# Optimization experiments

Hardware: AMD Instinct MI355X
Metric: run time of the kernel (lower is better)

The kernel has to match this reference:

```python
import jax, jax.numpy as jnp
import numpy as np

B, S, H = 4, 1024, 1024
NH, HD = 16, 64
SCALE = 1.0 / np.sqrt(HD)
VERB_BIAS, ROOT_BIAS, SUFFIX_BIAS = 2.0, 1.5, 1.2
BIG = np.float32(1e9)


def setup_inputs() -> dict:
    key = jax.random.key(0)
    ks = jax.random.split(key, 10)
    inp = {
        "hidden_states": jax.random.normal(ks[0], (B, S, H), dtype=jnp.float32),
        "morpho_types": jax.random.randint(ks[1], (B, S), 0, 5, dtype=jnp.int32),
        # torch Linear: y = x @ W.T + b; store W already transposed as [in, out]
        "Wq": jax.random.normal(ks[2], (H, H), dtype=jnp.float32) * 0.02,
        "bq": jnp.zeros((H,), dtype=jnp.float32),
        "Wk": jax.random.normal(ks[3], (H, H), dtype=jnp.float32) * 0.02,
        "bk": jnp.zeros((H,), dtype=jnp.float32),
        "Wv": jax.random.normal(ks[4], (H, H), dtype=jnp.float32) * 0.02,
        "bv": jnp.zeros((H,), dtype=jnp.float32),
        "Wo": jax.random.normal(ks[5], (H, H), dtype=jnp.float32) * 0.02,
        "bo": jnp.zeros((H,), dtype=jnp.float32),
    }
    return inp


def _morpho_bias(morpho_types):
    """Vectorized equivalent of _create_morpho_bias_mask. Returns [B, S, S]
    (the torch version broadcasts the same bias over all heads)."""
    is_verb = morpho_types == 2                      # [B, S]
    pos = jnp.arange(S)
    dist = jnp.abs(pos[:, None] - pos[None, :])      # [S, S]
    # mask non-verb columns with a huge distance; argmin ties -> smallest j,
    # matching torch's argmin over ascending verb_positions
    dist_m = jnp.where(is_verb[:, None, :], dist[None], BIG)  # [B, S, S]
    nearest = jnp.argmin(dist_m, axis=-1)            # [B, S]
    has_verb = jnp.any(is_verb, axis=-1)             # [B]
    verb_term = VERB_BIAS * jax.nn.one_hot(nearest, S, dtype=jnp.float32)
    verb_term = verb_term * has_verb[:, None, None].astype(jnp.float32)
    col_bias = (ROOT_BIAS * 0.5) * (morpho_types == 0).astype(jnp.float32) \
             + (SUFFIX_BIAS * 0.3) * (morpho_types == 1).astype(jnp.float32)  # [B, S]
    return verb_term + col_bias[:, None, :]          # [B, S, S]


def reference(hidden_states, morpho_types, Wq, bq, Wk, bk, Wv, bv, Wo, bo):
    def proj(W, b):
        y = hidden_states @ W + b                    # [B, S, H]
        return y.reshape(B, S, NH, HD).transpose(0, 2, 1, 3)  # [B, NH, S, HD]

    q = proj(Wq, bq)
    k = proj(Wk, bk)
    v = proj(Wv, bv)

    scores = jnp.einsum('bhqd,bhkd->bhqk', q, k) * SCALE   # [B, NH, S, S]
    scores = scores + _morpho_bias(morpho_types)[:, None]  # broadcast heads

    attn = jax.nn.softmax(scores, axis=-1)
    out = jnp.einsum('bhqk,bhkd->bhqd', attn, v)           # [B, NH, S, HD]
    out = out.transpose(0, 2, 1, 3).reshape(B, S, H)
    return out @ Wo + bo
```

## Files before the change

### kernel.cpp

```cpp
#include <hip/hip_runtime.h>


#define QSCALE 0.18033688011112042f
#define CB0    1.0820212806667225f
#define CB1    0.5193702147200268f
#define VERB2  2.8853900817779268f

typedef float  f32x4   __attribute__((ext_vector_type(4)));
typedef short  s16x8   __attribute__((ext_vector_type(8)));
typedef unsigned short u16x4 __attribute__((ext_vector_type(4)));
typedef unsigned short u16x8 __attribute__((ext_vector_type(8)));

#if __has_builtin(__builtin_amdgcn_exp2f)
#define EXP2F(x) __builtin_amdgcn_exp2f(x)
#else
#define EXP2F(x) exp2f(x)
#endif

__device__ __forceinline__ unsigned short f2bf(float f) {
  union { float f; unsigned u; } a; a.f = f;
  unsigned r = a.u + 0x7fffu + ((a.u >> 16) & 1u);
  return (unsigned short)(r >> 16);
}

__device__ __forceinline__ void async16(const void* g, void* l) {
  __builtin_amdgcn_global_load_lds(
      (const __attribute__((address_space(1))) unsigned int*)g,
      (__attribute__((address_space(3))) unsigned int*)l, 16, 0, 0);
}

__global__ __launch_bounds__(256) void k_prep(
    const float* __restrict__ hs, unsigned short* __restrict__ hsb,
    const float* __restrict__ Wq, const float* __restrict__ Wk,
    const float* __restrict__ Wv, const float* __restrict__ Wo,
    unsigned short* __restrict__ Wt, const int* __restrict__ mt,
    float* __restrict__ colbias, int* __restrict__ nearest) {
  __shared__ float t[64 * 68];
  int bx = blockIdx.x, tid = threadIdx.x;
  if (bx < 2048) {
    int i = (bx * 256 + tid) * 8;
    float4 v0 = *(const float4*)(hs + i);
    float4 v1 = *(const float4*)(hs + i + 4);
    u16x8 o;
    o[0] = f2bf(v0.x); o[1] = f2bf(v0.y); o[2] = f2bf(v0.z); o[3] = f2bf(v0.w);
    o[4] = f2bf(v1.x); o[5] = f2bf(v1.y); o[6] = f2bf(v1.z); o[7] = f2bf(v1.w);
    *(u16x8*)(hsb + i) = o;
  } else if (bx < 3072) {
    int w = (bx - 2048) >> 8, tt = (bx - 2048) & 255;
    const float* W = (w == 0) ? Wq : (w == 1) ? Wk : (w == 2) ? Wv : Wo;
    unsigned short* Wd = Wt + (size_t)w * 1048576;
    int n0 = (tt & 15) * 64, k0 = (tt >> 4) * 64;
    int r = tid >> 2, c0 = (tid & 3) * 16;
    const float* src = &W[(k0 + r) * 1024 + n0 + c0];
    float4 a0 = *(const float4*)(src + 0);
    float4 a1 = *(const float4*)(src + 4);
    float4 a2 = *(const float4*)(src + 8);
    float4 a3 = *(const float4*)(src + 12);
    *(float4*)&t[r * 68 + c0 + 0]  = a0;
    *(float4*)&t[r * 68 + c0 + 4]  = a1;
    *(float4*)&t[r * 68 + c0 + 8]  = a2;
    *(float4*)&t[r * 68 + c0 + 12] = a3;
    __syncthreads();
    u16x8 o0, o1;
#pragma unroll
    for (int j = 0; j < 8; j++) {
      o0[j] = f2bf(t[(c0 + j) * 68 + r]);
      o1[j] = f2bf(t[(c0 + 8 + j) * 68 + r]);
    }
    *(u16x8*)&Wd[(n0 + r) * 1024 + k0 + c0]     = o0;
    *(u16x8*)&Wd[(n0 + r) * 1024 + k0 + c0 + 8] = o1;
  } else {
    int i = bx - 3072;
    int b = i >> 2;
    int* sm = (int*)t;
    for (int j = tid; j < 1024; j += 256) sm[j] = mt[b * 1024 + j];
    __syncthreads();
    int q = (i & 3) * 256 + tid;
    int best = 1 << 30, bj = -1;
    for (int j = 0; j < 1024; ++j) {
      int d = (q > j) ? (q - j) : (j - q);
      int dd = (sm[j] == 2) ? d : (1 << 30);
      if (dd < best) { best = dd; bj = j; }
    }
    nearest[b * 1024 + q] = bj;
    int m = sm[q];
    colbias[b * 1024 + q] = CB0 * (m == 0) + CB1 * (m == 1);
  }
}

template <int MODE>
__global__ __launch_bounds__(256) void k_gemm(
    const unsigned short* __restrict__ A,
    const unsigned short* __restrict__ WtBase,
    const float* __restrict__ bias0, const float* __restrict__ bias1,
    const float* __restrict__ bias2,
    unsigned short* __restrict__ outB, unsigned short* __restrict__ outV,
    float* __restrict__ outF) {
  constexpr int TM = (MODE == 0) ? 128 : 64;
  constexpr int NI = (MODE == 0) ? 4 : 2;
  constexpr int RA = TM / 4;
  __shared__ unsigned short As[TM * 64];
  __shared__ unsigned short Bs[128 * 64];
  int tid = threadIdx.x, wid = tid >> 6, lane = tid & 63;
  int c = lane & 15, quad = lane >> 4;
  int m0, wsel, n0;
  const unsigned short* Bt;
  const float* bias;
  if (MODE == 0) {
    wsel = blockIdx.x >> 3;
    n0 = (blockIdx.x & 7) * 128;
    m0 = blockIdx.y * 128;
    Bt = WtBase + wsel * 1048576;
    bias = (wsel == 0) ? bias0 : ((wsel == 1) ? bias1 : bias2);
  } else {
    wsel = 0;
    n0 = blockIdx.x * 128;
    m0 = blockIdx.y * 64;
    Bt = WtBase; bias = bias0;
  }
  int wm = (wid >> 1) * (16 * NI), wn = (wid & 1) * 64;
  int lr = lane >> 3, lc = lane & 7;
  int gcol = ((lc ^ lr) << 3);
  const unsigned short* ga = A  + (size_t)(m0 + wid * RA + lr) * 1024 + gcol;
  const unsigned short* gb = Bt + (size_t)(n0 + wid * 32 + lr) * 1024 + gcol;
  unsigned short* lA = &As[(wid * RA) * 64];
  unsigned short* lB = &Bs[(wid * 32) * 64];

  f32x4 acc[NI][4];
#pragma unroll
  for (int i = 0; i < NI; i++)
#pragma unroll
    for (int j = 0; j < 4; j++) acc[i][j] = (f32x4){0.f, 0.f, 0.f, 0.f};

  bool sw = (MODE == 1) || (wsel != 2);

  for (int k0 = 0; k0 < 1024; k0 += 64) {
#pragma unroll
    for (int i = 0; i < RA / 8; i++) async16(ga + i * 8 * 1024 + k0, lA + i * 8 * 64);
#pragma unroll
    for (int j = 0; j < 4; j++)      async16(gb + j * 8 * 1024 + k0, lB + j * 8 * 64);
    __syncthreads();
#pragma unroll
    for (int ks = 0; ks < 2; ks++) {
      s16x8 af[NI], bf[4];
#pragma unroll
      for (int i = 0; i < NI; i++)
        af[i] = *(const s16x8*)&As[(wm + i * 16 + c) * 64 + (((ks * 4 + quad) ^ (c & 7)) << 3)];
#pragma unroll
      for (int j = 0; j < 4; j++)
        bf[j] = *(const s16x8*)&Bs[(wn + j * 16 + c) * 64 + (((ks * 4 + quad) ^ (c & 7)) << 3)];
      if (sw) {
#pragma unroll
        for (int i = 0; i < NI; i++)
#pragma unroll
          for (int j = 0; j < 4; j++)
            acc[i][j] = __builtin_amdgcn_mfma_f32_16x16x32_bf16(bf[j], af[i], acc[i][j], 0, 0, 0);
      } else {
#pragma unroll
        for (int i = 0; i < NI; i++)
#pragma unroll
          for (int j = 0; j < 4; j++)
            acc[i][j] = __builtin_amdgcn_mfma_f32_16x16x32_bf16(af[i], bf[j], acc[i][j], 0, 0, 0);
      }
    }
    __syncthreads();
  }

  if (MODE == 1) {
#pragma unroll
    for (int j = 0; j < 4; j++) {
      int colb = n0 + wn + j * 16 + quad * 4;
      f32x4 bvv = *(const f32x4*)&bias[colb];
#pragma unroll
      for (int i = 0; i < NI; i++) {
        int s_tok = m0 + wm + i * 16 + c;
        f32x4 v = acc[i][j] + bvv;
        *(f32x4*)&outF[(size_t)s_tok * 1024 + colb] = v;
      }
    }
  } else if (wsel == 2) {
#pragma unroll
    for (int j = 0; j < 4; j++) {
      int col = n0 + wn + j * 16 + c;
      float bv = bias[col];
      int h = col >> 6, d = col & 63;
#pragma unroll
      for (int i = 0; i < NI; i++) {
        int row = m0 + wm + i * 16 + quad * 4;
        int bb = row >> 10, s = row & 1023;
        u16x4 pk;
#pragma unroll
        for (int r = 0; r < 4; r++) pk[r] = f2bf(acc[i][j][r] + bv);
        *(u16x4*)&outV[(size_t)(((bb * 16 + h) * 64 + d)) * 1024 + s] = pk;
      }
    }
  } else {
    float sc = (wsel == 0) ? QSCALE : 1.0f;
#pragma unroll
    for (int j = 0; j < 4; j++) {
      int colb = n0 + wn + j * 16 + quad * 4;
      f32x4 bvv = *(const f32x4*)&bias[colb];
      int h = colb >> 6, d0 = colb & 63;
#pragma unroll
      for (int i = 0; i < NI; i++) {
        int s_tok = m0 + wm + i * 16 + c;
        int bb = s_tok >> 10, s = s_tok & 1023;
        u16x4 pk;
#pragma unroll
        for (int r = 0; r < 4; r++) pk[r] = f2bf((acc[i][j][r] + bvv[r]) * sc);
        *(u16x4*)&outB[(size_t)wsel * 4194304 + (((bb * 16 + h) * 1024 + s) * 64) + d0] = pk;
      }
    }
  }
}

__global__ __launch_bounds__(256) void k_attn(
    const unsigned short* __restrict__ Q, const unsigned short* __restrict__ K,
    const unsigned short* __restrict__ Vt, const float* __restrict__ colbias,
    const int* __restrict__ nearest, unsigned short* __restrict__ AO) {
  __shared__ unsigned short Ks[64 * 72];
  __shared__ unsigned short Vs[64 * 72];
  __shared__ unsigned short Ps[4][16 * 72];
  __shared__ float Cb[1024];
  int tid = threadIdx.x, wid = tid >> 6, lane = tid & 63;
  int c = lane & 15, quad = lane >> 4;
  int bh = blockIdx.x, qt = blockIdx.y;
  int b = bh >> 4, head = bh & 15;
  int q0 = qt * 64, wq = wid * 16;
  const unsigned short* Qg = Q  + (size_t)(bh * 1024 + q0 + wq) * 64;
  const unsigned short* Kg = K  + (size_t)bh * 1024 * 64;
  const unsigned short* Vg = Vt + (size_t)bh * 64 * 1024;

  *(float4*)&Cb[tid * 4] = *(const float4*)&colbias[b * 1024 + tid * 4];

  s16x8 qf[2];
#pragma unroll
  for (int ks = 0; ks < 2; ks++)
    qf[ks] = *(const s16x8*)&Qg[c * 64 + ks * 32 + quad * 8];

  int nq = nearest[b * 1024 + q0 + wq + c];

  f32x4 o[4];
#pragma unroll
  for (int j = 0; j < 4; j++) o[j] = (f32x4){0.f, 0.f, 0.f, 0.f};
  float lrun = 0.f;

  int srow = tid >> 3, scol8 = (tid & 7) * 8;

  u16x8 kr[2], vr[2];
#pragma unroll
  for (int it = 0; it < 2; ++it) {
    int r2 = it * 32 + srow;
    kr[it] = *(const u16x8*)&Kg[r2 * 64 + scol8];
    vr[it] = *(const u16x8*)&Vg[r2 * 1024 + scol8];
  }
  __syncthreads();

  for (int kc = 0; kc < 16; ++kc) {
#pragma unroll
    for (int it = 0; it < 2; ++it) {
      int r2 = it * 32 + srow;
      *(u16x8*)&Ks[r2 * 72 + scol8] = kr[it];
      *(u16x8*)&Vs[r2 * 72 + scol8] = vr[it];
    }
    __syncthreads();
    if (kc < 15) {
#pragma unroll
      for (int it = 0; it < 2; ++it) {
        int r2 = it * 32 + srow;
        kr[it] = *(const u16x8*)&Kg[((kc + 1) * 64 + r2) * 64 + scol8];
        vr[it] = *(const u16x8*)&Vg[r2 * 1024 + (kc + 1) * 64 + scol8];
      }
    }

    f32x4 st[4];
#pragma unroll
    for (int mt = 0; mt < 4; mt++) st[mt] = (f32x4){0.f, 0.f, 0.f, 0.f};
#pragma unroll
    for (int mt = 0; mt < 4; mt++)
#pragma unroll
      for (int ks = 0; ks < 2; ks++) {
        s16x8 a = *(const s16x8*)&Ks[(mt * 16 + c) * 72 + ks * 32 + quad * 8];
        st[mt] = __builtin_amdgcn_mfma_f32_16x16x32_bf16(a, qf[ks], st[mt], 0, 0, 0);
      }

    if (__any((nq >> 6) == kc)) {
#pragma unroll
      for (int mt = 0; mt < 4; mt++)
#pragma unroll
        for (int r = 0; r < 4; r++)
          if (kc * 64 + mt * 16 + quad * 4 + r == nq) st[mt][r] += VERB2;
    }

#pragma unroll
    for (int mt = 0; mt < 4; mt++) {
      f32x4 cb = *(const f32x4*)&Cb[kc * 64 + mt * 16 + quad * 4];
      float e0 = EXP2F(st[mt][0] + cb[0]);
      float e1 = EXP2F(st[mt][1] + cb[1]);
      float e2 = EXP2F(st[mt][2] + cb[2]);
      float e3 = EXP2F(st[mt][3] + cb[3]);
      unsigned p01 = __builtin_amdgcn_perm(__float_as_uint(e1), __float_as_uint(e0), 0x07060302u);
      unsigned p23 = __builtin_amdgcn_perm(__float_as_uint(e3), __float_as_uint(e2), 0x07060302u);
      lrun += __uint_as_float(p01 << 16) + __uint_as_float(p01 & 0xffff0000u)
            + __uint_as_float(p23 << 16) + __uint_as_float(p23 & 0xffff0000u);
      uint2 pk; pk.x = p01; pk.y = p23;
      *(uint2*)&Ps[wid][c * 72 + mt * 16 + quad * 4] = pk;
    }
    __asm__ volatile("s_waitcnt lgkmcnt(0)" ::: "memory");

#pragma unroll
    for (int ks = 0; ks < 2; ks++) {
      s16x8 pa = *(const s16x8*)&Ps[wid][c * 72 + ks * 32 + quad * 8];
#pragma unroll
      for (int ntd = 0; ntd < 4; ntd++) {
        s16x8 vb = *(const s16x8*)&Vs[(ntd * 16 + c) * 72 + ks * 32 + quad * 8];
        o[ntd] = __builtin_amdgcn_mfma_f32_16x16x32_bf16(vb, pa, o[ntd], 0, 0, 0);
      }
    }
    __syncthreads();
  }

  lrun += __shfl_xor(lrun, 16, 64);
  lrun += __shfl_xor(lrun, 32, 64);
  float linv = 1.0f / lrun;
  size_t row = (size_t)(b * 1024 + q0 + wq + c);
#pragma unroll
  for (int ntd = 0; ntd < 4; ntd++) {
    int d0 = ntd * 16 + quad * 4;
    u16x4 pk;
#pragma unroll
    for (int r = 0; r < 4; r++) pk[r] = f2bf(o[ntd][r] * linv);
    *(u16x4*)&AO[row * 1024 + head * 64 + d0] = pk;
  }
}

extern "C" void kernel_launch(void* const* d_in, const int* in_sizes, int n_in,
                              void* d_out, int out_size, void* d_ws, size_t ws_size,
                              hipStream_t stream) {
  const float* hs     = (const float*)d_in[0];
  const int*   morpho = (const int*)d_in[1];
  const float* Wq = (const float*)d_in[2];
  const float* bq = (const float*)d_in[3];
  const float* Wk = (const float*)d_in[4];
  const float* bk = (const float*)d_in[5];
  const float* Wv = (const float*)d_in[6];
  const float* bv = (const float*)d_in[7];
  const float* Wo = (const float*)d_in[8];
  const float* bo = (const float*)d_in[9];
  float* out = (float*)d_out;

  char* ws = (char*)d_ws;
  unsigned short* hsb = (unsigned short*)(ws);
  unsigned short* Wt  = (unsigned short*)(ws + (8u << 20));
  unsigned short* Qb  = (unsigned short*)(ws + (16u << 20));
  unsigned short* Kb  = (unsigned short*)(ws + (24u << 20));
  unsigned short* Vtb = (unsigned short*)(ws + (40u << 20));
  float* colbias      = (float*)(ws + (48u << 20));
  int*   nearestp     = (int*)(ws + (48u << 20) + (16u << 10));
  unsigned short* AO  = hsb;

  k_prep<<<3088, 256, 0, stream>>>(hs, hsb, Wq, Wk, Wv, Wo, Wt, morpho,
                                   colbias, nearestp);
  k_gemm<0><<<dim3(24, 32), 256, 0, stream>>>(hsb, Wt, bq, bk, bv, Qb, Vtb, nullptr);
  k_attn<<<dim3(64, 16), 256, 0, stream>>>(Qb, Kb, Vtb, colbias, nearestp, AO);
  k_gemm<1><<<dim3(8, 64), 256, 0, stream>>>(AO, Wt + 3 * 1048576, bo, nullptr, nullptr,
                                             nullptr, nullptr, out);
  (void)in_sizes; (void)n_in; (void)out_size; (void)ws_size; (void)Kb;
}
```

Baseline: 211.5 us.

## Double-buffer K/V LDS tiles in attention and stage output GEMM stores through LDS

The attention kernel now keeps two LDS buffers for K and V. Each iteration writes the next chunk into the alternate buffer and prefetches the chunk after that into registers, which drops the barrier that used to sit between the LDS store and the compute. The output-projection GEMM epilogue now transposes its accumulator tile through XOR-swizzled shared memory, so each wave writes full contiguous 256-byte rows to global memory instead of scattered 16-byte pieces. This costs more LDS for attention, which may lower occupancy. The single end-of-loop barrier must still protect the buffer being overwritten, and the rotation is subtle.

```diff
diff --git a/kernel.cpp b/kernel.cpp
--- a/kernel.cpp
+++ b/kernel.cpp
@@ -99,8 +99,9 @@
   constexpr int TM = (MODE == 0) ? 128 : 64;
   constexpr int NI = (MODE == 0) ? 4 : 2;
   constexpr int RA = TM / 4;
-  __shared__ unsigned short As[TM * 64];
-  __shared__ unsigned short Bs[128 * 64];
+  __shared__ unsigned short SMEM[16384];
+  unsigned short* As = SMEM;
+  unsigned short* Bs = SMEM + TM * 64;
   int tid = threadIdx.x, wid = tid >> 6, lane = tid & 63;
   int c = lane & 15, quad = lane >> 4;
   int m0, wsel, n0;
@@ -167,16 +168,27 @@
   }
 
   if (MODE == 1) {
+    float* Wf = (float*)SMEM + wid * 2048;
 #pragma unroll
     for (int j = 0; j < 4; j++) {
       int colb = n0 + wn + j * 16 + quad * 4;
       f32x4 bvv = *(const f32x4*)&bias[colb];
 #pragma unroll
       for (int i = 0; i < NI; i++) {
-        int s_tok = m0 + wm + i * 16 + c;
         f32x4 v = acc[i][j] + bvv;
-        *(f32x4*)&outF[(size_t)s_tok * 1024 + colb] = v;
-      }
+        int tokl = i * 16 + c;
+        int chs = (j * 4 + quad) ^ c;
+        *(f32x4*)&Wf[tokl * 64 + chs * 4] = v;
+      }
+    }
+    __asm__ volatile("s_waitcnt lgkmcnt(0)" ::: "memory");
+    int t4 = lane >> 4, chl = lane & 15;
+#pragma unroll
+    for (int t = 0; t < 8; t++) {
+      int tokl = t * 4 + t4;
+      int chs = chl ^ (tokl & 15);
+      f32x4 v = *(const f32x4*)&Wf[tokl * 64 + chs * 4];
+      *(f32x4*)&outF[(size_t)(m0 + wm + tokl) * 1024 + n0 + wn + chl * 4] = v;
     }
   } else if (wsel == 2) {
 #pragma unroll
@@ -218,8 +230,8 @@
     const unsigned short* __restrict__ Q, const unsigned short* __restrict__ K,
     const unsigned short* __restrict__ Vt, const float* __restrict__ colbias,
     const int* __restrict__ nearest, unsigned short* __restrict__ AO) {
-  __shared__ unsigned short Ks[64 * 72];
-  __shared__ unsigned short Vs[64 * 72];
+  __shared__ unsigned short Ks[2][64 * 72];
+  __shared__ unsigned short Vs[2][64 * 72];
   __shared__ unsigned short Ps[4][16 * 72];
   __shared__ float Cb[1024];
   int tid = threadIdx.x, wid = tid >> 6, lane = tid & 63;
@@ -254,22 +266,36 @@
     kr[it] = *(const u16x8*)&Kg[r2 * 64 + scol8];
     vr[it] = *(const u16x8*)&Vg[r2 * 1024 + scol8];
   }
+#pragma unroll
+  for (int it = 0; it < 2; ++it) {
+    int r2 = it * 32 + srow;
+    *(u16x8*)&Ks[0][r2 * 72 + scol8] = kr[it];
+    *(u16x8*)&Vs[0][r2 * 72 + scol8] = vr[it];
+  }
+#pragma unroll
+  for (int it = 0; it < 2; ++it) {
+    int r2 = it * 32 + srow;
+    kr[it] = *(const u16x8*)&Kg[(64 + r2) * 64 + scol8];
+    vr[it] = *(const u16x8*)&Vg[r2 * 1024 + 64 + scol8];
+  }
   __syncthreads();
 
   for (int kc = 0; kc < 16; ++kc) {
-#pragma unroll
-    for (int it = 0; it < 2; ++it) {
-      int r2 = it * 32 + srow;
-      *(u16x8*)&Ks[r2 * 72 + scol8] = kr[it];
-      *(u16x8*)&Vs[r2 * 72 + scol8] = vr[it];
-    }
-    __syncthreads();
+    int cur = kc & 1;
     if (kc < 15) {
 #pragma unroll
       for (int it = 0; it < 2; ++it) {
         int r2 = it * 32 + srow;
-        kr[it] = *(const u16x8*)&Kg[((kc + 1) * 64 + r2) * 64 + scol8];
-        vr[it] = *(const u16x8*)&Vg[r2 * 1024 + (kc + 1) * 64 + scol8];
+        *(u16x8*)&Ks[cur ^ 1][r2 * 72 + scol8] = kr[it];
+        *(u16x8*)&Vs[cur ^ 1][r2 * 72 + scol8] = vr[it];
+      }
+    }
+    if (kc < 14) {
+#pragma unroll
+      for (int it = 0; it < 2; ++it) {
+        int r2 = it * 32 + srow;
+        kr[it] = *(const u16x8*)&Kg[((kc + 2) * 64 + r2) * 64 + scol8];
+        vr[it] = *(const u16x8*)&Vg[r2 * 1024 + (kc + 2) * 64 + scol8];
       }
     }
 
@@ -280,7 +306,7 @@
     for (int mt = 0; mt < 4; mt++)
 #pragma unroll
       for (int ks = 0; ks < 2; ks++) {
-        s16x8 a = *(const s16x8*)&Ks[(mt * 16 + c) * 72 + ks * 32 + quad * 8];
+        s16x8 a = *(const s16x8*)&Ks[cur][(mt * 16 + c) * 72 + ks * 32 + quad * 8];
         st[mt] = __builtin_amdgcn_mfma_f32_16x16x32_bf16(a, qf[ks], st[mt], 0, 0, 0);
       }
 
@@ -313,7 +339,7 @@
       s16x8 pa = *(const s16x8*)&Ps[wid][c * 72 + ks * 32 + quad * 8];
 #pragma unroll
       for (int ntd = 0; ntd < 4; ntd++) {
-        s16x8 vb = *(const s16x8*)&Vs[(ntd * 16 + c) * 72 + ks * 32 + quad * 8];
+        s16x8 vb = *(const s16x8*)&Vs[cur][(ntd * 16 + c) * 72 + ks * 32 + quad * 8];
         o[ntd] = __builtin_amdgcn_mfma_f32_16x16x32_bf16(vb, pa, o[ntd], 0, 0, 0);
       }
     }
```

Result: no change. 214.6 us (+1.5%).

## Double-buffer K/V shared tiles with XOR swizzle in attention kernel

Applied to the files above, without the earlier changes.

The attention kernel now keeps two shared-memory buffers for K and V tiles. The next tile is written to the alternate buffer while the current one is consumed, which removes the store-then-barrier step at the top of each iteration, and global loads are prefetched two chunks ahead. Row padding (stride 72) is replaced by an XOR swizzle on 8-element chunks for K, V and P to avoid LDS bank conflicts without padding. The cost is more LDS per block and more register lifetime for prefetched data, which may lower occupancy.

```diff
diff --git a/kernel.cpp b/kernel.cpp
--- a/kernel.cpp
+++ b/kernel.cpp
@@ -218,9 +218,9 @@
     const unsigned short* __restrict__ Q, const unsigned short* __restrict__ K,
     const unsigned short* __restrict__ Vt, const float* __restrict__ colbias,
     const int* __restrict__ nearest, unsigned short* __restrict__ AO) {
-  __shared__ unsigned short Ks[64 * 72];
-  __shared__ unsigned short Vs[64 * 72];
-  __shared__ unsigned short Ps[4][16 * 72];
+  __shared__ unsigned short Ks[2][64 * 64];
+  __shared__ unsigned short Vs[2][64 * 64];
+  __shared__ unsigned short Ps[4][16 * 64];
   __shared__ float Cb[1024];
   int tid = threadIdx.x, wid = tid >> 6, lane = tid & 63;
   int c = lane & 15, quad = lane >> 4;
@@ -245,7 +245,10 @@
   for (int j = 0; j < 4; j++) o[j] = (f32x4){0.f, 0.f, 0.f, 0.f};
   float lrun = 0.f;
 
-  int srow = tid >> 3, scol8 = (tid & 7) * 8;
+  int srow = tid >> 3;
+  int swz8 = (((tid & 7) ^ (srow & 7)) << 3);
+  int scol8 = (tid & 7) * 8;
+  const int cs = c & 7;
 
   u16x8 kr[2], vr[2];
 #pragma unroll
@@ -254,22 +257,36 @@
     kr[it] = *(const u16x8*)&Kg[r2 * 64 + scol8];
     vr[it] = *(const u16x8*)&Vg[r2 * 1024 + scol8];
   }
+#pragma unroll
+  for (int it = 0; it < 2; ++it) {
+    int r2 = it * 32 + srow;
+    *(u16x8*)&Ks[0][r2 * 64 + swz8] = kr[it];
+    *(u16x8*)&Vs[0][r2 * 64 + swz8] = vr[it];
+  }
+#pragma unroll
+  for (int it = 0; it < 2; ++it) {
+    int r2 = it * 32 + srow;
+    kr[it] = *(const u16x8*)&Kg[(64 + r2) * 64 + scol8];
+    vr[it] = *(const u16x8*)&Vg[r2 * 1024 + 64 + scol8];
+  }
   __syncthreads();
 
   for (int kc = 0; kc < 16; ++kc) {
-#pragma unroll
-    for (int it = 0; it < 2; ++it) {
-      int r2 = it * 32 + srow;
-      *(u16x8*)&Ks[r2 * 72 + scol8] = kr[it];
-      *(u16x8*)&Vs[r2 * 72 + scol8] = vr[it];
-    }
-    __syncthreads();
+    int cur = kc & 1;
     if (kc < 15) {
 #pragma unroll
       for (int it = 0; it < 2; ++it) {
         int r2 = it * 32 + srow;
-        kr[it] = *(const u16x8*)&Kg[((kc + 1) * 64 + r2) * 64 + scol8];
-        vr[it] = *(const u16x8*)&Vg[r2 * 1024 + (kc + 1) * 64 + scol8];
+        *(u16x8*)&Ks[cur ^ 1][r2 * 64 + swz8] = kr[it];
+        *(u16x8*)&Vs[cur ^ 1][r2 * 64 + swz8] = vr[it];
+      }
+    }
+    if (kc < 14) {
+#pragma unroll
+      for (int it = 0; it < 2; ++it) {
+        int r2 = it * 32 + srow;
+        kr[it] = *(const u16x8*)&Kg[((kc + 2) * 64 + r2) * 64 + scol8];
+        vr[it] = *(const u16x8*)&Vg[r2 * 1024 + (kc + 2) * 64 + scol8];
       }
     }
 
@@ -280,7 +297,7 @@
     for (int mt = 0; mt < 4; mt++)
 #pragma unroll
       for (int ks = 0; ks < 2; ks++) {
-        s16x8 a = *(const s16x8*)&Ks[(mt * 16 + c) * 72 + ks * 32 + quad * 8];
+        s16x8 a = *(const s16x8*)&Ks[cur][(mt * 16 + c) * 64 + (((ks * 4 + quad) ^ cs) << 3)];
         st[mt] = __builtin_amdgcn_mfma_f32_16x16x32_bf16(a, qf[ks], st[mt], 0, 0, 0);
       }
 
@@ -304,16 +321,17 @@
       lrun += __uint_as_float(p01 << 16) + __uint_as_float(p01 & 0xffff0000u)
             + __uint_as_float(p23 << 16) + __uint_as_float(p23 & 0xffff0000u);
       uint2 pk; pk.x = p01; pk.y = p23;
-      *(uint2*)&Ps[wid][c * 72 + mt * 16 + quad * 4] = pk;
+      int chs = (2 * mt + (quad >> 1)) ^ cs;
+      *(uint2*)&Ps[wid][c * 64 + chs * 8 + (quad & 1) * 4] = pk;
     }
     __asm__ volatile("s_waitcnt lgkmcnt(0)" ::: "memory");
 
 #pragma unroll
     for (int ks = 0; ks < 2; ks++) {
-      s16x8 pa = *(const s16x8*)&Ps[wid][c * 72 + ks * 32 + quad * 8];
+      s16x8 pa = *(const s16x8*)&Ps[wid][c * 64 + (((ks * 4 + quad) ^ cs) << 3)];
 #pragma unroll
       for (int ntd = 0; ntd < 4; ntd++) {
-        s16x8 vb = *(const s16x8*)&Vs[(ntd * 16 + c) * 72 + ks * 32 + quad * 8];
+        s16x8 vb = *(const s16x8*)&Vs[cur][(ntd * 16 + c) * 64 + (((ks * 4 + quad) ^ cs) << 3)];
         o[ntd] = __builtin_amdgcn_mfma_f32_16x16x32_bf16(vb, pa, o[ntd], 0, 0, 0);
       }
     }
```

Result: no change. 211.8 us (+0.1%).
